# Optimization experiments

Measured on AMD Instinct MI355X. Metric: run time of the kernel, lower is better.

Reference implementation:

```python
import jax, jax.numpy as jnp
import numpy as np

# Dimensions (match init_kwargs / input_specs)
B, CIN, COUT = 4, 8, 32
HIN, WIN = 721, 1440      # input (nlat, nlon)
HOUT, WOUT = 361, 720     # output (nlat, nlon)
K = 9                     # morlet basis: kernel_shape[0]*kernel_shape[1]
NNZ = 32                  # nonzeros per (basis fn, output-lat) row of sparse psi
PSCALE = WIN // WOUT      # longitudinal downsampling factor (must be integer)


def setup_inputs() -> dict:
    key = jax.random.key(0)
    k1, k2, k3, k4, k5 = jax.random.split(key, 5)
    x = jax.random.normal(k1, (B, CIN, HIN, WIN), jnp.float32)
    # Localized sparse support: input lat rows near the matching output lat
    # (emulates the theta_cutoff neighborhood of the precomputed DISCO tensor).
    base_row = jnp.round(jnp.arange(HOUT) * (HIN - 1) / (HOUT - 1)).astype(jnp.int32)
    drow = jax.random.randint(k2, (K, HOUT, NNZ), -2, 3)
    rows = jnp.clip(base_row[None, :, None] + drow, 0, HIN - 1)
    # small longitudinal offsets; the contraction shifts them over all output lons
    cols = jax.random.randint(k3, (K, HOUT, NNZ), 0, 16)
    psi_idx = (rows * WIN + cols).astype(jnp.int32)          # [K, HOUT, NNZ]
    psi_vals = jax.random.normal(k4, (K, HOUT, NNZ), jnp.float32) / NNZ
    weight = jax.random.normal(k5, (COUT, CIN, K), jnp.float32) / np.sqrt(CIN * K)
    return {"x": x, "psi_idx": psi_idx, "psi_vals": psi_vals, "weight": weight}


def _disco_conv(x, psi_idx, psi_vals, weight):
    # DISCO S2 contraction (dense math of torch_harmonics _disco_s2_contraction):
    #   out[b,o,xo,po] = sum_{c,k} weight[o,c,k] * y[b,c,k,xo,po]
    Bv, C, Hin, Win = x.shape
    rows = psi_idx // Win               # [K, Hout, NNZ]
    cols = psi_idx % Win
    x_flat = x.reshape(Bv, C, Hin * Win)

    def step(_, po):
        cols_p = (cols + po * PSCALE) % Win
        idx = rows * Win + cols_p                        # [K,Hout,NNZ]
        xg = x_flat[:, :, idx]                           # [B,C,K,Hout,NNZ] gather
        y_po = jnp.einsum('bckxn,kxn->bckx', xg, psi_vals)
        return None, y_po

    _, y = jax.lax.scan(step, None, jnp.arange(WOUT))    # [Wout,B,C,K,Hout]
    out = jnp.einsum('pbckx,ock->boxp', y, weight)       # [B,Cout,Hout,Wout]
    return out


def reference(x, psi_idx, psi_vals, weight):
    # The wrapper only casts to float32 around the conv; inputs are already fp32.
    return _disco_conv(x.astype(jnp.float32), psi_idx, psi_vals, weight)
```

## Files before the change

kernel.cpp:

```cpp
#include <hip/hip_runtime.h>
#include <hip/hip_bf16.h>

#define HIN   721
#define WIN   1440
#define HOUT_ 361
#define WOUT_ 720
#define NB    4
#define CIN_  8
#define COUT_ 32
#define KT    9
#define NNZ_  32

typedef short  bsh8   __attribute__((ext_vector_type(8)));
typedef float  f32x16 __attribute__((ext_vector_type(16)));
typedef unsigned int u32x4 __attribute__((ext_vector_type(4)));

static __device__ __forceinline__ unsigned short f2bf(float f) {
  unsigned u = __builtin_bit_cast(unsigned, f);
  u += 0x7fffu + ((u >> 16) & 1u);
  return (unsigned short)(u >> 16);
}

static __device__ __forceinline__ unsigned pack2(float a, float b) {
  __hip_bfloat162 h = __float22bfloat162_rn(make_float2(a, b));
  unsigned u; __builtin_memcpy(&u, &h, 4);
  return u;
}

__global__ __launch_bounds__(256) void coeff_kernel(
    const int*   __restrict__ psi_idx,
    const float* __restrict__ psi_vals,
    const float* __restrict__ weight,
    unsigned short* __restrict__ Cg)
{
  __shared__ float Cl[256 * 81];
  __shared__ float wl[COUT_ * CIN_ * KT];
  __shared__ float S[KT][80];

  const int x = blockIdx.x, tid = threadIdx.x;

  for (int i = tid; i < KT * 80; i += 256) ((float*)S)[i] = 0.f;
  for (int i = tid; i < COUT_ * CIN_ * KT; i += 256) wl[i] = weight[i];
  __syncthreads();

  for (int i = tid; i < KT * NNZ_; i += 256) {
    int k = i >> 5, n = i & 31;
    int gi  = (k * HOUT_ + x) * NNZ_ + n;
    int idx = psi_idx[gi];
    int r   = idx / WIN;
    int col = idx - r * WIN;
    int s   = r - 2 * x + 2;
    int slot = (s * 2 + (col & 1)) * 8 + (col >> 1);
    atomicAdd(&S[k][slot], psi_vals[gi]);
  }
  __syncthreads();

  {
    const float* wrow = &wl[tid * KT];
    float w[KT];
    #pragma unroll
    for (int k = 0; k < KT; ++k) w[k] = wrow[k];
    float* seg = &Cl[tid * 81];
    #pragma unroll
    for (int slot = 0; slot < 80; ++slot) {
      float acc = 0.f;
      #pragma unroll
      for (int k = 0; k < KT; ++k) acc += w[k] * S[k][slot];
      seg[slot] = acc;
    }
  }
  __syncthreads();

  for (int chunk = tid; chunk < 8 * 10 * 32; chunk += 256) {
    int j   = chunk / 320;
    int rem = chunk - j * 320;
    int qb  = rem >> 5, o = rem & 31;
    u32x4 pack;
    #pragma unroll
    for (int h = 0; h < 4; ++h) {
      int q0 = qb * 8 + 2 * h;
      int c0 = q0 / 10, ql0 = q0 - c0 * 10;
      int q1 = q0 + 1;
      int c1 = q1 / 10, ql1 = q1 - c1 * 10;
      unsigned lo = f2bf(Cl[(o * CIN_ + c0) * 81 + ql0 * 8 + j]);
      unsigned hi = f2bf(Cl[(o * CIN_ + c1) * 81 + ql1 * 8 + j]);
      pack[h] = lo | (hi << 16);
    }
    *(u32x4*)&Cg[((size_t)x * 2560 + (size_t)((j * 10 + qb) * 32 + o)) * 8] = pack;
  }
}

#define PB   256
#define ROWS 264
#define RST  176

__global__ __launch_bounds__(256, 3) void disco_main_kernel(
    const float* __restrict__ x,
    const unsigned short* __restrict__ Cg,
    float* __restrict__ out)
{
  __shared__ __align__(16) unsigned char Ut[ROWS * RST];

  const int g   = blockIdx.x;
  const int xcd = g & 7, lin = g >> 3;
  const int swz = (xcd < 4) ? xcd * 542 + lin : 4 * 542 + (xcd - 4) * 541 + lin;
  const int xo  = swz / 12;
  const int rem = swz - xo * 12;
  const int pt  = rem % 3;
  const int b   = rem / 3;
  const int p0  = pt * PB;
  const int tid = threadIdx.x;

  const int lane = tid & 63;
  const int wv   = tid >> 6;
  const int half = lane >> 5;
  const int l31  = lane & 31;
  const int wbase = wv * 64;

  const unsigned short* cgx = Cg + (size_t)xo * 2560 * 8
                                 + (size_t)(half * 32 + l31) * 8;

  bsh8 a0[5], a1[5];
  #pragma unroll
  for (int kb = 0; kb < 5; ++kb) a0[kb] = *(const bsh8*)&cgx[kb * 512];
  #pragma unroll
  for (int kb = 0; kb < 5; ++kb) a1[kb] = *(const bsh8*)&cgx[2560 + kb * 512];

  const float* xb = x + (size_t)b * (CIN_ * HIN * WIN);

  int rr[5];
  #pragma unroll
  for (int s = 0; s < 5; ++s) {
    int r = 2 * xo + s - 2;
    rr[s] = r < 0 ? 0 : (r > HIN - 1 ? HIN - 1 : r);
  }

  #pragma unroll
  for (int bp = 0; bp < 2; ++bp) {
    float4 v0[4], v1[4];
    const int uA = tid + (2 * bp) * 256, uB = uA + 256;
    const int chA = uA / 132, rpA = uA - chA * 132;
    const int chB = uB / 132, rpB = uB - chB * 132;
    int cwA = p0 + 2 * rpA; if (cwA >= WOUT_) cwA -= WOUT_;
    int cwB = p0 + 2 * rpB; if (cwB >= WOUT_) cwB -= WOUT_;
    #pragma unroll
    for (int m = 0; m < 4; ++m) {
      int qpA = 4 * chA + m, cA = (qpA * 205) >> 10, sA = qpA - cA * 5;
      v0[m] = *(const float4*)&xb[(size_t)(cA * HIN + rr[sA]) * WIN + 2 * cwA];
      int qpB = 4 * chB + m, cB = (qpB * 205) >> 10, sB = qpB - cB * 5;
      v1[m] = *(const float4*)&xb[(size_t)(cB * HIN + rr[sB]) * WIN + 2 * cwB];
    }
    u32x4 lo, hi;
    #pragma unroll
    for (int m = 0; m < 4; ++m) { lo[m] = pack2(v0[m].x, v0[m].y); hi[m] = pack2(v0[m].z, v0[m].w); }
    int byte0 = (2 * rpA) * RST + chA * 16;
    *(u32x4*)&Ut[byte0]       = lo;
    *(u32x4*)&Ut[byte0 + RST] = hi;
    #pragma unroll
    for (int m = 0; m < 4; ++m) { lo[m] = pack2(v1[m].x, v1[m].y); hi[m] = pack2(v1[m].z, v1[m].w); }
    byte0 = (2 * rpB) * RST + chB * 16;
    *(u32x4*)&Ut[byte0]       = lo;
    *(u32x4*)&Ut[byte0 + RST] = hi;
  }
  {
    const int uA = tid + 1024;
    const int chA = uA / 132, rpA = uA - chA * 132;
    int cwA = p0 + 2 * rpA; if (cwA >= WOUT_) cwA -= WOUT_;
    float4 v0[4], v1[4];
    int chB = 0, rpB = 0;
    const bool tail = tid < 40;
    if (tail) {
      const int uB = tid + 1280;
      chB = uB / 132; rpB = uB - chB * 132;
    }
    int cwB = p0 + 2 * rpB; if (cwB >= WOUT_) cwB -= WOUT_;
    #pragma unroll
    for (int m = 0; m < 4; ++m) {
      int qpA = 4 * chA + m, cA = (qpA * 205) >> 10, sA = qpA - cA * 5;
      v0[m] = *(const float4*)&xb[(size_t)(cA * HIN + rr[sA]) * WIN + 2 * cwA];
    }
    if (tail) {
      #pragma unroll
      for (int m = 0; m < 4; ++m) {
        int qpB = 4 * chB + m, cB = (qpB * 205) >> 10, sB = qpB - cB * 5;
        v1[m] = *(const float4*)&xb[(size_t)(cB * HIN + rr[sB]) * WIN + 2 * cwB];
      }
    }
    u32x4 lo, hi;
    #pragma unroll
    for (int m = 0; m < 4; ++m) { lo[m] = pack2(v0[m].x, v0[m].y); hi[m] = pack2(v0[m].z, v0[m].w); }
    int byte0 = (2 * rpA) * RST + chA * 16;
    *(u32x4*)&Ut[byte0]       = lo;
    *(u32x4*)&Ut[byte0 + RST] = hi;
    if (tail) {
      #pragma unroll
      for (int m = 0; m < 4; ++m) { lo[m] = pack2(v1[m].x, v1[m].y); hi[m] = pack2(v1[m].z, v1[m].w); }
      byte0 = (2 * rpB) * RST + chB * 16;
      *(u32x4*)&Ut[byte0]       = lo;
      *(u32x4*)&Ut[byte0 + RST] = hi;
    }
  }
  __syncthreads();

  f32x16 acc0 = {};
  f32x16 acc1 = {};

  #pragma unroll
  for (int j = 0; j < 8; ++j) {
    bsh8 a2[5];
    if (j < 6) {
      #pragma unroll
      for (int kb = 0; kb < 5; ++kb)
        a2[kb] = *(const bsh8*)&cgx[(j + 2) * 2560 + kb * 512];
    }
    const int row0 = wbase + l31 + j;
    const int rb0  = row0 * RST;
    const int rb1  = rb0 + 32 * RST;
    #pragma unroll
    for (int kb = 0; kb < 5; ++kb) {
      const int cho = (2 * kb + half) * 16;
      bsh8 b0 = *(const bsh8*)&Ut[rb0 + cho];
      acc0 = __builtin_amdgcn_mfma_f32_32x32x16_bf16(a0[kb], b0, acc0, 0, 0, 0);
      bsh8 b1 = *(const bsh8*)&Ut[rb1 + cho];
      acc1 = __builtin_amdgcn_mfma_f32_32x32x16_bf16(a0[kb], b1, acc1, 0, 0, 0);
    }
    #pragma unroll
    for (int kb = 0; kb < 5; ++kb) { a0[kb] = a1[kb]; a1[kb] = a2[kb]; }
  }

  const int p = p0 + wbase + l31;
  #pragma unroll
  for (int r = 0; r < 16; ++r) {
    int o = (r & 3) + 8 * (r >> 2) + 4 * half;
    size_t base = ((size_t)(b * COUT_ + o) * HOUT_ + xo) * WOUT_;
    if (p < WOUT_)
      __builtin_nontemporal_store(acc0[r], &out[base + p]);
    if (p + 32 < WOUT_)
      __builtin_nontemporal_store(acc1[r], &out[base + p + 32]);
  }
}

extern "C" void kernel_launch(void* const* d_in, const int* in_sizes, int n_in,
                              void* d_out, int out_size, void* d_ws, size_t ws_size,
                              hipStream_t stream) {
  const float* x        = (const float*)d_in[0];
  const int*   psi_idx  = (const int*)d_in[1];
  const float* psi_vals = (const float*)d_in[2];
  const float* weight   = (const float*)d_in[3];
  float* out = (float*)d_out;
  unsigned short* Cg = (unsigned short*)d_ws;

  coeff_kernel<<<dim3(HOUT_), 256, 0, stream>>>(psi_idx, psi_vals, weight, Cg);
  disco_main_kernel<<<dim3(3 * NB * HOUT_), 256, 0, stream>>>(x, Cg, out);
}
```

Measured before the change: 93.33 us.

## Split LDS staging into two phases to overlap global loads with MFMA

Splits the K dimension of the staged tile into two parts. The first three k-blocks (channels 0-5) are loaded and stored to LDS, then the loads for the remaining channels are issued before the first MFMA loop, so their global latency hides behind compute. The second half is packed into LDS after the first loop, followed by a barrier and a second MFMA loop. This costs an extra barrier and keeps more loaded values in registers across the first loop, which may hurt occupancy at the 3-blocks-per-SM launch bound.

```diff
diff --git a/kernel.cpp b/kernel.cpp
--- a/kernel.cpp
+++ b/kernel.cpp
@@ -120,11 +120,11 @@
   const unsigned short* cgx = Cg + (size_t)xo * 2560 * 8
                                  + (size_t)(half * 32 + l31) * 8;
 
-  bsh8 a0[5], a1[5];
-  #pragma unroll
-  for (int kb = 0; kb < 5; ++kb) a0[kb] = *(const bsh8*)&cgx[kb * 512];
-  #pragma unroll
-  for (int kb = 0; kb < 5; ++kb) a1[kb] = *(const bsh8*)&cgx[2560 + kb * 512];
+  bsh8 a0[3], a1[3];
+  #pragma unroll
+  for (int kb = 0; kb < 3; ++kb) a0[kb] = *(const bsh8*)&cgx[kb * 512];
+  #pragma unroll
+  for (int kb = 0; kb < 3; ++kb) a1[kb] = *(const bsh8*)&cgx[2560 + kb * 512];
 
   const float* xb = x + (size_t)b * (CIN_ * HIN * WIN);
 
@@ -135,71 +135,92 @@
     rr[s] = r < 0 ? 0 : (r > HIN - 1 ? HIN - 1 : r);
   }
 
-  #pragma unroll
-  for (int bp = 0; bp < 2; ++bp) {
-    float4 v0[4], v1[4];
-    const int uA = tid + (2 * bp) * 256, uB = uA + 256;
-    const int chA = uA / 132, rpA = uA - chA * 132;
-    const int chB = uB / 132, rpB = uB - chB * 132;
-    int cwA = p0 + 2 * rpA; if (cwA >= WOUT_) cwA -= WOUT_;
-    int cwB = p0 + 2 * rpB; if (cwB >= WOUT_) cwB -= WOUT_;
-    #pragma unroll
-    for (int m = 0; m < 4; ++m) {
-      int qpA = 4 * chA + m, cA = (qpA * 205) >> 10, sA = qpA - cA * 5;
-      v0[m] = *(const float4*)&xb[(size_t)(cA * HIN + rr[sA]) * WIN + 2 * cwA];
-      int qpB = 4 * chB + m, cB = (qpB * 205) >> 10, sB = qpB - cB * 5;
-      v1[m] = *(const float4*)&xb[(size_t)(cB * HIN + rr[sB]) * WIN + 2 * cwB];
-    }
-    u32x4 lo, hi;
-    #pragma unroll
-    for (int m = 0; m < 4; ++m) { lo[m] = pack2(v0[m].x, v0[m].y); hi[m] = pack2(v0[m].z, v0[m].w); }
-    int byte0 = (2 * rpA) * RST + chA * 16;
-    *(u32x4*)&Ut[byte0]       = lo;
-    *(u32x4*)&Ut[byte0 + RST] = hi;
-    #pragma unroll
-    for (int m = 0; m < 4; ++m) { lo[m] = pack2(v1[m].x, v1[m].y); hi[m] = pack2(v1[m].z, v1[m].w); }
-    byte0 = (2 * rpB) * RST + chB * 16;
-    *(u32x4*)&Ut[byte0]       = lo;
-    *(u32x4*)&Ut[byte0 + RST] = hi;
-  }
   {
-    const int uA = tid + 1024;
-    const int chA = uA / 132, rpA = uA - chA * 132;
-    int cwA = p0 + 2 * rpA; if (cwA >= WOUT_) cwA -= WOUT_;
-    float4 v0[4], v1[4];
-    int chB = 0, rpB = 0;
-    const bool tail = tid < 40;
-    if (tail) {
-      const int uB = tid + 1280;
-      chB = uB / 132; rpB = uB - chB * 132;
-    }
-    int cwB = p0 + 2 * rpB; if (cwB >= WOUT_) cwB -= WOUT_;
-    #pragma unroll
-    for (int m = 0; m < 4; ++m) {
-      int qpA = 4 * chA + m, cA = (qpA * 205) >> 10, sA = qpA - cA * 5;
-      v0[m] = *(const float4*)&xb[(size_t)(cA * HIN + rr[sA]) * WIN + 2 * cwA];
-    }
-    if (tail) {
+    float4 v[3][4];
+    #pragma unroll
+    for (int pass = 0; pass < 3; ++pass) {
+      const int u  = tid + pass * 256;
+      const int ch = u / 132, rp = u - ch * 132;
+      int cw = p0 + 2 * rp; if (cw >= WOUT_) cw -= WOUT_;
       #pragma unroll
       for (int m = 0; m < 4; ++m) {
-        int qpB = 4 * chB + m, cB = (qpB * 205) >> 10, sB = qpB - cB * 5;
-        v1[m] = *(const float4*)&xb[(size_t)(cB * HIN + rr[sB]) * WIN + 2 * cwB];
+        int qp = 4 * ch + m, c = (qp * 205) >> 10, s = qp - c * 5;
+        v[pass][m] = *(const float4*)&xb[(size_t)(c * HIN + rr[s]) * WIN + 2 * cw];
       }
     }
-    u32x4 lo, hi;
-    #pragma unroll
-    for (int m = 0; m < 4; ++m) { lo[m] = pack2(v0[m].x, v0[m].y); hi[m] = pack2(v0[m].z, v0[m].w); }
-    int byte0 = (2 * rpA) * RST + chA * 16;
-    *(u32x4*)&Ut[byte0]       = lo;
-    *(u32x4*)&Ut[byte0 + RST] = hi;
-    if (tail) {
-      #pragma unroll
-      for (int m = 0; m < 4; ++m) { lo[m] = pack2(v1[m].x, v1[m].y); hi[m] = pack2(v1[m].z, v1[m].w); }
-      byte0 = (2 * rpB) * RST + chB * 16;
+    float4 vt[4];
+    const bool tailA = tid < 24;
+    {
+      const int u  = tailA ? (768 + tid) : 768;
+      const int ch = u / 132, rp = u - ch * 132;
+      int cw = p0 + 2 * rp; if (cw >= WOUT_) cw -= WOUT_;
+      if (tailA) {
+        #pragma unroll
+        for (int m = 0; m < 4; ++m) {
+          int qp = 4 * ch + m, c = (qp * 205) >> 10, s = qp - c * 5;
+          vt[m] = *(const float4*)&xb[(size_t)(c * HIN + rr[s]) * WIN + 2 * cw];
+        }
+      }
+    }
+    #pragma unroll
+    for (int pass = 0; pass < 3; ++pass) {
+      const int u  = tid + pass * 256;
+      const int ch = u / 132, rp = u - ch * 132;
+      u32x4 lo, hi;
+      #pragma unroll
+      for (int m = 0; m < 4; ++m) { lo[m] = pack2(v[pass][m].x, v[pass][m].y);
+                                    hi[m] = pack2(v[pass][m].z, v[pass][m].w); }
+      int byte0 = (2 * rp) * RST + ch * 16;
       *(u32x4*)&Ut[byte0]       = lo;
       *(u32x4*)&Ut[byte0 + RST] = hi;
     }
-  }
+    if (tailA) {
+      const int u  = 768 + tid;
+      const int ch = u / 132, rp = u - ch * 132;
+      u32x4 lo, hi;
+      #pragma unroll
+      for (int m = 0; m < 4; ++m) { lo[m] = pack2(vt[m].x, vt[m].y);
+                                    hi[m] = pack2(vt[m].z, vt[m].w); }
+      int byte0 = (2 * rp) * RST + ch * 16;
+      *(u32x4*)&Ut[byte0]       = lo;
+      *(u32x4*)&Ut[byte0 + RST] = hi;
+    }
+  }
+
+  float4 vB[2][4], vBt[4];
+  int uB[2], uBt;
+  const bool tailB = tid < 16;
+  #pragma unroll
+  for (int pass = 0; pass < 2; ++pass) {
+    const int u  = 792 + tid + pass * 256;
+    uB[pass] = u;
+    const int ch = u / 132, rp = u - ch * 132;
+    int cw = p0 + 2 * rp; if (cw >= WOUT_) cw -= WOUT_;
+    #pragma unroll
+    for (int m = 0; m < 4; ++m) {
+      int qp = 4 * ch + m, c = (qp * 205) >> 10, s = qp - c * 5;
+      vB[pass][m] = *(const float4*)&xb[(size_t)(c * HIN + rr[s]) * WIN + 2 * cw];
+    }
+  }
+  {
+    uBt = tailB ? (1304 + tid) : 1304;
+    const int ch = uBt / 132, rp = uBt - ch * 132;
+    int cw = p0 + 2 * rp; if (cw >= WOUT_) cw -= WOUT_;
+    if (tailB) {
+      #pragma unroll
+      for (int m = 0; m < 4; ++m) {
+        int qp = 4 * ch + m, c = (qp * 205) >> 10, s = qp - c * 5;
+        vBt[m] = *(const float4*)&xb[(size_t)(c * HIN + rr[s]) * WIN + 2 * cw];
+      }
+    }
+  }
+
+  bsh8 c0[2], c1[2];
+  #pragma unroll
+  for (int i = 0; i < 2; ++i) c0[i] = *(const bsh8*)&cgx[(3 + i) * 512];
+  #pragma unroll
+  for (int i = 0; i < 2; ++i) c1[i] = *(const bsh8*)&cgx[2560 + (3 + i) * 512];
+
   __syncthreads();
 
   f32x16 acc0 = {};
@@ -207,17 +228,16 @@
 
   #pragma unroll
   for (int j = 0; j < 8; ++j) {
-    bsh8 a2[5];
+    bsh8 a2[3];
     if (j < 6) {
       #pragma unroll
-      for (int kb = 0; kb < 5; ++kb)
+      for (int kb = 0; kb < 3; ++kb)
         a2[kb] = *(const bsh8*)&cgx[(j + 2) * 2560 + kb * 512];
     }
-    const int row0 = wbase + l31 + j;
-    const int rb0  = row0 * RST;
-    const int rb1  = rb0 + 32 * RST;
-    #pragma unroll
-    for (int kb = 0; kb < 5; ++kb) {
+    const int rb0 = (wbase + l31 + j) * RST;
+    const int rb1 = rb0 + 32 * RST;
+    #pragma unroll
+    for (int kb = 0; kb < 3; ++kb) {
       const int cho = (2 * kb + half) * 16;
       bsh8 b0 = *(const bsh8*)&Ut[rb0 + cho];
       acc0 = __builtin_amdgcn_mfma_f32_32x32x16_bf16(a0[kb], b0, acc0, 0, 0, 0);
@@ -225,7 +245,53 @@
       acc1 = __builtin_amdgcn_mfma_f32_32x32x16_bf16(a0[kb], b1, acc1, 0, 0, 0);
     }
     #pragma unroll
-    for (int kb = 0; kb < 5; ++kb) { a0[kb] = a1[kb]; a1[kb] = a2[kb]; }
+    for (int kb = 0; kb < 3; ++kb) { a0[kb] = a1[kb]; a1[kb] = a2[kb]; }
+  }
+
+  #pragma unroll
+  for (int pass = 0; pass < 2; ++pass) {
+    const int u  = uB[pass];
+    const int ch = u / 132, rp = u - ch * 132;
+    u32x4 lo, hi;
+    #pragma unroll
+    for (int m = 0; m < 4; ++m) { lo[m] = pack2(vB[pass][m].x, vB[pass][m].y);
+                                  hi[m] = pack2(vB[pass][m].z, vB[pass][m].w); }
+    int byte0 = (2 * rp) * RST + ch * 16;
+    *(u32x4*)&Ut[byte0]       = lo;
+    *(u32x4*)&Ut[byte0 + RST] = hi;
+  }
+  if (tailB) {
+    const int ch = uBt / 132, rp = uBt - ch * 132;
+    u32x4 lo, hi;
+    #pragma unroll
+    for (int m = 0; m < 4; ++m) { lo[m] = pack2(vBt[m].x, vBt[m].y);
+                                  hi[m] = pack2(vBt[m].z, vBt[m].w); }
+    int byte0 = (2 * rp) * RST + ch * 16;
+    *(u32x4*)&Ut[byte0]       = lo;
+    *(u32x4*)&Ut[byte0 + RST] = hi;
+  }
+  __syncthreads();
+
+  #pragma unroll
+  for (int j = 0; j < 8; ++j) {
+    bsh8 c2[2];
+    if (j < 6) {
+      #pragma unroll
+      for (int i = 0; i < 2; ++i)
+        c2[i] = *(const bsh8*)&cgx[(j + 2) * 2560 + (3 + i) * 512];
+    }
+    const int rb0 = (wbase + l31 + j) * RST;
+    const int rb1 = rb0 + 32 * RST;
+    #pragma unroll
+    for (int i = 0; i < 2; ++i) {
+      const int cho = (6 + 2 * i + half) * 16;
+      bsh8 b0 = *(const bsh8*)&Ut[rb0 + cho];
+      acc0 = __builtin_amdgcn_mfma_f32_32x32x16_bf16(c0[i], b0, acc0, 0, 0, 0);
+      bsh8 b1 = *(const bsh8*)&Ut[rb1 + cho];
+      acc1 = __builtin_amdgcn_mfma_f32_32x32x16_bf16(c0[i], b1, acc1, 0, 0, 0);
+    }
+    #pragma unroll
+    for (int i = 0; i < 2; ++i) { c0[i] = c1[i]; c1[i] = c2[i]; }
   }
 
   const int p = p0 + wbase + l31;
```

Result: slower. 96.34 us (+3.2%).

## Shrink main kernel to single-wave blocks with private LDS tile, drop barrier

Applied to the files above, without the earlier changes.

Restructures the main kernel from 256-thread blocks covering 256 output longitudes to 64-thread single-wave blocks covering 64 longitudes, each staging its own 72-row bf16 tile in LDS. Because only one wave touches the tile, the block-wide barrier is removed and more, smaller blocks can overlap loads and MFMA across the CU. In exchange, the 8-row halo is reloaded per wave instead of being shared across four waves, which adds redundant global traffic, and the launch has four times as many blocks. The grid swizzle assumes 17328 blocks split evenly across 8 XCDs. Removing the barrier relies on the wave executing its LDS stores and loads in order.

```diff
diff --git a/kernel.cpp b/kernel.cpp
--- a/kernel.cpp
+++ b/kernel.cpp
@@ -90,32 +90,28 @@
   }
 }
 
-#define PB   256
-#define ROWS 264
-#define RST  176
-
-__global__ __launch_bounds__(256, 3) void disco_main_kernel(
+#define WROWS 72
+#define RST   176
+
+__global__ __launch_bounds__(64, 3) void disco_main_kernel(
     const float* __restrict__ x,
     const unsigned short* __restrict__ Cg,
     float* __restrict__ out)
 {
-  __shared__ __align__(16) unsigned char Ut[ROWS * RST];
+  __shared__ __align__(16) unsigned char Ut[WROWS * RST];
 
   const int g   = blockIdx.x;
   const int xcd = g & 7, lin = g >> 3;
-  const int swz = (xcd < 4) ? xcd * 542 + lin : 4 * 542 + (xcd - 4) * 541 + lin;
-  const int xo  = swz / 12;
-  const int rem = swz - xo * 12;
-  const int pt  = rem % 3;
-  const int b   = rem / 3;
-  const int p0  = pt * PB;
-  const int tid = threadIdx.x;
-
-  const int lane = tid & 63;
-  const int wv   = tid >> 6;
+  const int swz = xcd * 2166 + lin;
+  const int xo  = swz / 48;
+  const int rem = swz - xo * 48;
+  const int b   = rem / 12;
+  const int pw  = rem - b * 12;
+  const int po  = pw * 64;
+
+  const int lane = threadIdx.x;
   const int half = lane >> 5;
   const int l31  = lane & 31;
-  const int wbase = wv * 64;
 
   const unsigned short* cgx = Cg + (size_t)xo * 2560 * 8
                                  + (size_t)(half * 32 + l31) * 8;
@@ -135,72 +131,80 @@
     rr[s] = r < 0 ? 0 : (r > HIN - 1 ? HIN - 1 : r);
   }
 
-  #pragma unroll
-  for (int bp = 0; bp < 2; ++bp) {
-    float4 v0[4], v1[4];
-    const int uA = tid + (2 * bp) * 256, uB = uA + 256;
-    const int chA = uA / 132, rpA = uA - chA * 132;
-    const int chB = uB / 132, rpB = uB - chB * 132;
-    int cwA = p0 + 2 * rpA; if (cwA >= WOUT_) cwA -= WOUT_;
-    int cwB = p0 + 2 * rpB; if (cwB >= WOUT_) cwB -= WOUT_;
-    #pragma unroll
-    for (int m = 0; m < 4; ++m) {
-      int qpA = 4 * chA + m, cA = (qpA * 205) >> 10, sA = qpA - cA * 5;
-      v0[m] = *(const float4*)&xb[(size_t)(cA * HIN + rr[sA]) * WIN + 2 * cwA];
-      int qpB = 4 * chB + m, cB = (qpB * 205) >> 10, sB = qpB - cB * 5;
-      v1[m] = *(const float4*)&xb[(size_t)(cB * HIN + rr[sB]) * WIN + 2 * cwB];
-    }
-    u32x4 lo, hi;
-    #pragma unroll
-    for (int m = 0; m < 4; ++m) { lo[m] = pack2(v0[m].x, v0[m].y); hi[m] = pack2(v0[m].z, v0[m].w); }
-    int byte0 = (2 * rpA) * RST + chA * 16;
-    *(u32x4*)&Ut[byte0]       = lo;
-    *(u32x4*)&Ut[byte0 + RST] = hi;
-    #pragma unroll
-    for (int m = 0; m < 4; ++m) { lo[m] = pack2(v1[m].x, v1[m].y); hi[m] = pack2(v1[m].z, v1[m].w); }
-    byte0 = (2 * rpB) * RST + chB * 16;
-    *(u32x4*)&Ut[byte0]       = lo;
-    *(u32x4*)&Ut[byte0 + RST] = hi;
-  }
   {
-    const int uA = tid + 1024;
-    const int chA = uA / 132, rpA = uA - chA * 132;
-    int cwA = p0 + 2 * rpA; if (cwA >= WOUT_) cwA -= WOUT_;
-    float4 v0[4], v1[4];
-    int chB = 0, rpB = 0;
-    const bool tail = tid < 40;
-    if (tail) {
-      const int uB = tid + 1280;
-      chB = uB / 132; rpB = uB - chB * 132;
-    }
-    int cwB = p0 + 2 * rpB; if (cwB >= WOUT_) cwB -= WOUT_;
-    #pragma unroll
-    for (int m = 0; m < 4; ++m) {
-      int qpA = 4 * chA + m, cA = (qpA * 205) >> 10, sA = qpA - cA * 5;
-      v0[m] = *(const float4*)&xb[(size_t)(cA * HIN + rr[sA]) * WIN + 2 * cwA];
-    }
-    if (tail) {
+    float4 v[3][4];
+    #pragma unroll
+    for (int k = 0; k < 3; ++k) {
+      const int u  = lane + k * 64;
+      const int ch = u / 36, rp = u - ch * 36;
+      int cw = po + 2 * rp; if (cw >= WOUT_) cw -= WOUT_;
       #pragma unroll
       for (int m = 0; m < 4; ++m) {
-        int qpB = 4 * chB + m, cB = (qpB * 205) >> 10, sB = qpB - cB * 5;
-        v1[m] = *(const float4*)&xb[(size_t)(cB * HIN + rr[sB]) * WIN + 2 * cwB];
+        int qp = 4 * ch + m, c = (qp * 205) >> 10, s = qp - c * 5;
+        v[k][m] = *(const float4*)&xb[(size_t)(c * HIN + rr[s]) * WIN + 2 * cw];
       }
     }
-    u32x4 lo, hi;
-    #pragma unroll
-    for (int m = 0; m < 4; ++m) { lo[m] = pack2(v0[m].x, v0[m].y); hi[m] = pack2(v0[m].z, v0[m].w); }
-    int byte0 = (2 * rpA) * RST + chA * 16;
-    *(u32x4*)&Ut[byte0]       = lo;
-    *(u32x4*)&Ut[byte0 + RST] = hi;
-    if (tail) {
-      #pragma unroll
-      for (int m = 0; m < 4; ++m) { lo[m] = pack2(v1[m].x, v1[m].y); hi[m] = pack2(v1[m].z, v1[m].w); }
-      byte0 = (2 * rpB) * RST + chB * 16;
+    #pragma unroll
+    for (int k = 0; k < 3; ++k) {
+      const int u  = lane + k * 64;
+      const int ch = u / 36, rp = u - ch * 36;
+      u32x4 lo, hi;
+      #pragma unroll
+      for (int m = 0; m < 4; ++m) { lo[m] = pack2(v[k][m].x, v[k][m].y);
+                                    hi[m] = pack2(v[k][m].z, v[k][m].w); }
+      const int byte0 = (2 * rp) * RST + ch * 16;
       *(u32x4*)&Ut[byte0]       = lo;
       *(u32x4*)&Ut[byte0 + RST] = hi;
     }
   }
-  __syncthreads();
+  {
+    float4 v[2][4], vt[4];
+    const bool tl = lane < 40;
+    #pragma unroll
+    for (int k = 0; k < 2; ++k) {
+      const int u  = lane + (3 + k) * 64;
+      const int ch = u / 36, rp = u - ch * 36;
+      int cw = po + 2 * rp; if (cw >= WOUT_) cw -= WOUT_;
+      #pragma unroll
+      for (int m = 0; m < 4; ++m) {
+        int qp = 4 * ch + m, c = (qp * 205) >> 10, s = qp - c * 5;
+        v[k][m] = *(const float4*)&xb[(size_t)(c * HIN + rr[s]) * WIN + 2 * cw];
+      }
+    }
+    if (tl) {
+      const int u  = 320 + lane;
+      const int ch = u / 36, rp = u - ch * 36;
+      int cw = po + 2 * rp; if (cw >= WOUT_) cw -= WOUT_;
+      #pragma unroll
+      for (int m = 0; m < 4; ++m) {
+        int qp = 4 * ch + m, c = (qp * 205) >> 10, s = qp - c * 5;
+        vt[m] = *(const float4*)&xb[(size_t)(c * HIN + rr[s]) * WIN + 2 * cw];
+      }
+    }
+    #pragma unroll
+    for (int k = 0; k < 2; ++k) {
+      const int u  = lane + (3 + k) * 64;
+      const int ch = u / 36, rp = u - ch * 36;
+      u32x4 lo, hi;
+      #pragma unroll
+      for (int m = 0; m < 4; ++m) { lo[m] = pack2(v[k][m].x, v[k][m].y);
+                                    hi[m] = pack2(v[k][m].z, v[k][m].w); }
+      const int byte0 = (2 * rp) * RST + ch * 16;
+      *(u32x4*)&Ut[byte0]       = lo;
+      *(u32x4*)&Ut[byte0 + RST] = hi;
+    }
+    if (tl) {
+      const int u  = 320 + lane;
+      const int ch = u / 36, rp = u - ch * 36;
+      u32x4 lo, hi;
+      #pragma unroll
+      for (int m = 0; m < 4; ++m) { lo[m] = pack2(vt[m].x, vt[m].y);
+                                    hi[m] = pack2(vt[m].z, vt[m].w); }
+      const int byte0 = (2 * rp) * RST + ch * 16;
+      *(u32x4*)&Ut[byte0]       = lo;
+      *(u32x4*)&Ut[byte0 + RST] = hi;
+    }
+  }
 
   f32x16 acc0 = {};
   f32x16 acc1 = {};
@@ -213,9 +217,8 @@
       for (int kb = 0; kb < 5; ++kb)
         a2[kb] = *(const bsh8*)&cgx[(j + 2) * 2560 + kb * 512];
     }
-    const int row0 = wbase + l31 + j;
-    const int rb0  = row0 * RST;
-    const int rb1  = rb0 + 32 * RST;
+    const int rb0 = (l31 + j) * RST;
+    const int rb1 = rb0 + 32 * RST;
     #pragma unroll
     for (int kb = 0; kb < 5; ++kb) {
       const int cho = (2 * kb + half) * 16;
@@ -228,7 +231,7 @@
     for (int kb = 0; kb < 5; ++kb) { a0[kb] = a1[kb]; a1[kb] = a2[kb]; }
   }
 
-  const int p = p0 + wbase + l31;
+  const int p = po + l31;
   #pragma unroll
   for (int r = 0; r < 16; ++r) {
     int o = (r & 3) + 8 * (r >> 2) + 4 * half;
@@ -251,5 +254,5 @@
   unsigned short* Cg = (unsigned short*)d_ws;
 
   coeff_kernel<<<dim3(HOUT_), 256, 0, stream>>>(psi_idx, psi_vals, weight, Cg);
-  disco_main_kernel<<<dim3(3 * NB * HOUT_), 256, 0, stream>>>(x, Cg, out);
-}
+  disco_main_kernel<<<dim3(12 * NB * HOUT_), 64, 0, stream>>>(x, Cg, out);
+}
```

New measurement: 97.62 us. +4.6%, slower.

## Loop longitude tiles inside each block and shrink coeff kernel shared memory

Applied to the files above, without the earlier changes.

The main kernel now launches one block per (output latitude, batch) and runs the three longitude tiles in a loop inside the block, with a barrier between tiles that reuse the same LDS buffer. This cuts block count and launch/scheduling overhead, and lets repeated coefficient loads hit cache. The cost is fewer blocks and less parallelism, plus serialized tiles with no overlap of loads and MFMA. The coeff kernel also stores bf16 coefficients in LDS and reads weights straight into registers, shrinking shared memory so more blocks can be resident.

```diff
diff --git a/kernel.cpp b/kernel.cpp
--- a/kernel.cpp
+++ b/kernel.cpp
@@ -27,20 +27,18 @@
   return u;
 }
 
-__global__ __launch_bounds__(256) void coeff_kernel(
+__global__ __launch_bounds__(256, 3) void coeff_kernel(
     const int*   __restrict__ psi_idx,
     const float* __restrict__ psi_vals,
     const float* __restrict__ weight,
     unsigned short* __restrict__ Cg)
 {
-  __shared__ float Cl[256 * 81];
-  __shared__ float wl[COUT_ * CIN_ * KT];
+  __shared__ unsigned short Cl16[256 * 83];
   __shared__ float S[KT][80];
 
   const int x = blockIdx.x, tid = threadIdx.x;
 
   for (int i = tid; i < KT * 80; i += 256) ((float*)S)[i] = 0.f;
-  for (int i = tid; i < COUT_ * CIN_ * KT; i += 256) wl[i] = weight[i];
   __syncthreads();
 
   for (int i = tid; i < KT * NNZ_; i += 256) {
@@ -53,20 +51,20 @@
     int slot = (s * 2 + (col & 1)) * 8 + (col >> 1);
     atomicAdd(&S[k][slot], psi_vals[gi]);
   }
+
+  float w[KT];
+  #pragma unroll
+  for (int k = 0; k < KT; ++k) w[k] = weight[tid * KT + k];
   __syncthreads();
 
   {
-    const float* wrow = &wl[tid * KT];
-    float w[KT];
-    #pragma unroll
-    for (int k = 0; k < KT; ++k) w[k] = wrow[k];
-    float* seg = &Cl[tid * 81];
+    unsigned short* seg = &Cl16[tid * 83];
     #pragma unroll
     for (int slot = 0; slot < 80; ++slot) {
       float acc = 0.f;
       #pragma unroll
       for (int k = 0; k < KT; ++k) acc += w[k] * S[k][slot];
-      seg[slot] = acc;
+      seg[slot] = f2bf(acc);
     }
   }
   __syncthreads();
@@ -82,8 +80,8 @@
       int c0 = q0 / 10, ql0 = q0 - c0 * 10;
       int q1 = q0 + 1;
       int c1 = q1 / 10, ql1 = q1 - c1 * 10;
-      unsigned lo = f2bf(Cl[(o * CIN_ + c0) * 81 + ql0 * 8 + j]);
-      unsigned hi = f2bf(Cl[(o * CIN_ + c1) * 81 + ql1 * 8 + j]);
+      unsigned lo = Cl16[(o * CIN_ + c0) * 83 + ql0 * 8 + j];
+      unsigned hi = Cl16[(o * CIN_ + c1) * 83 + ql1 * 8 + j];
       pack[h] = lo | (hi << 16);
     }
     *(u32x4*)&Cg[((size_t)x * 2560 + (size_t)((j * 10 + qb) * 32 + o)) * 8] = pack;
@@ -103,12 +101,9 @@
 
   const int g   = blockIdx.x;
   const int xcd = g & 7, lin = g >> 3;
-  const int swz = (xcd < 4) ? xcd * 542 + lin : 4 * 542 + (xcd - 4) * 541 + lin;
-  const int xo  = swz / 12;
-  const int rem = swz - xo * 12;
-  const int pt  = rem % 3;
-  const int b   = rem / 3;
-  const int p0  = pt * PB;
+  const int swz = (xcd < 4) ? xcd * 181 + lin : 724 + (xcd - 4) * 180 + lin;
+  const int xo  = swz >> 2;
+  const int b   = swz & 3;
   const int tid = threadIdx.x;
 
   const int lane = tid & 63;
@@ -119,13 +114,6 @@
 
   const unsigned short* cgx = Cg + (size_t)xo * 2560 * 8
                                  + (size_t)(half * 32 + l31) * 8;
-
-  bsh8 a0[5], a1[5];
-  #pragma unroll
-  for (int kb = 0; kb < 5; ++kb) a0[kb] = *(const bsh8*)&cgx[kb * 512];
-  #pragma unroll
-  for (int kb = 0; kb < 5; ++kb) a1[kb] = *(const bsh8*)&cgx[2560 + kb * 512];
-
   const float* xb = x + (size_t)b * (CIN_ * HIN * WIN);
 
   int rr[5];
@@ -135,108 +123,118 @@
     rr[s] = r < 0 ? 0 : (r > HIN - 1 ? HIN - 1 : r);
   }
 
-  #pragma unroll
-  for (int bp = 0; bp < 2; ++bp) {
-    float4 v0[4], v1[4];
-    const int uA = tid + (2 * bp) * 256, uB = uA + 256;
-    const int chA = uA / 132, rpA = uA - chA * 132;
-    const int chB = uB / 132, rpB = uB - chB * 132;
-    int cwA = p0 + 2 * rpA; if (cwA >= WOUT_) cwA -= WOUT_;
-    int cwB = p0 + 2 * rpB; if (cwB >= WOUT_) cwB -= WOUT_;
-    #pragma unroll
-    for (int m = 0; m < 4; ++m) {
-      int qpA = 4 * chA + m, cA = (qpA * 205) >> 10, sA = qpA - cA * 5;
-      v0[m] = *(const float4*)&xb[(size_t)(cA * HIN + rr[sA]) * WIN + 2 * cwA];
-      int qpB = 4 * chB + m, cB = (qpB * 205) >> 10, sB = qpB - cB * 5;
-      v1[m] = *(const float4*)&xb[(size_t)(cB * HIN + rr[sB]) * WIN + 2 * cwB];
-    }
-    u32x4 lo, hi;
-    #pragma unroll
-    for (int m = 0; m < 4; ++m) { lo[m] = pack2(v0[m].x, v0[m].y); hi[m] = pack2(v0[m].z, v0[m].w); }
-    int byte0 = (2 * rpA) * RST + chA * 16;
-    *(u32x4*)&Ut[byte0]       = lo;
-    *(u32x4*)&Ut[byte0 + RST] = hi;
-    #pragma unroll
-    for (int m = 0; m < 4; ++m) { lo[m] = pack2(v1[m].x, v1[m].y); hi[m] = pack2(v1[m].z, v1[m].w); }
-    byte0 = (2 * rpB) * RST + chB * 16;
-    *(u32x4*)&Ut[byte0]       = lo;
-    *(u32x4*)&Ut[byte0 + RST] = hi;
-  }
-  {
-    const int uA = tid + 1024;
-    const int chA = uA / 132, rpA = uA - chA * 132;
-    int cwA = p0 + 2 * rpA; if (cwA >= WOUT_) cwA -= WOUT_;
-    float4 v0[4], v1[4];
-    int chB = 0, rpB = 0;
-    const bool tail = tid < 40;
-    if (tail) {
-      const int uB = tid + 1280;
-      chB = uB / 132; rpB = uB - chB * 132;
-    }
-    int cwB = p0 + 2 * rpB; if (cwB >= WOUT_) cwB -= WOUT_;
-    #pragma unroll
-    for (int m = 0; m < 4; ++m) {
-      int qpA = 4 * chA + m, cA = (qpA * 205) >> 10, sA = qpA - cA * 5;
-      v0[m] = *(const float4*)&xb[(size_t)(cA * HIN + rr[sA]) * WIN + 2 * cwA];
-    }
-    if (tail) {
+  for (int pt = 0; pt < 3; ++pt) {
+    const int p0 = pt * PB;
+    if (pt) __syncthreads();
+
+    bsh8 a0[5], a1[5];
+    #pragma unroll
+    for (int kb = 0; kb < 5; ++kb) a0[kb] = *(const bsh8*)&cgx[kb * 512];
+    #pragma unroll
+    for (int kb = 0; kb < 5; ++kb) a1[kb] = *(const bsh8*)&cgx[2560 + kb * 512];
+
+    #pragma unroll
+    for (int bp = 0; bp < 2; ++bp) {
+      float4 v0[4], v1[4];
+      const int uA = tid + (2 * bp) * 256, uB = uA + 256;
+      const int chA = uA / 132, rpA = uA - chA * 132;
+      const int chB = uB / 132, rpB = uB - chB * 132;
+      int cwA = p0 + 2 * rpA; if (cwA >= WOUT_) cwA -= WOUT_;
+      int cwB = p0 + 2 * rpB; if (cwB >= WOUT_) cwB -= WOUT_;
       #pragma unroll
       for (int m = 0; m < 4; ++m) {
+        int qpA = 4 * chA + m, cA = (qpA * 205) >> 10, sA = qpA - cA * 5;
+        v0[m] = *(const float4*)&xb[(size_t)(cA * HIN + rr[sA]) * WIN + 2 * cwA];
         int qpB = 4 * chB + m, cB = (qpB * 205) >> 10, sB = qpB - cB * 5;
         v1[m] = *(const float4*)&xb[(size_t)(cB * HIN + rr[sB]) * WIN + 2 * cwB];
       }
-    }
-    u32x4 lo, hi;
-    #pragma unroll
-    for (int m = 0; m < 4; ++m) { lo[m] = pack2(v0[m].x, v0[m].y); hi[m] = pack2(v0[m].z, v0[m].w); }
-    int byte0 = (2 * rpA) * RST + chA * 16;
-    *(u32x4*)&Ut[byte0]       = lo;
-    *(u32x4*)&Ut[byte0 + RST] = hi;
-    if (tail) {
+      u32x4 lo, hi;
+      #pragma unroll
+      for (int m = 0; m < 4; ++m) { lo[m] = pack2(v0[m].x, v0[m].y); hi[m] = pack2(v0[m].z, v0[m].w); }
+      int byte0 = (2 * rpA) * RST + chA * 16;
+      *(u32x4*)&Ut[byte0]       = lo;
+      *(u32x4*)&Ut[byte0 + RST] = hi;
       #pragma unroll
       for (int m = 0; m < 4; ++m) { lo[m] = pack2(v1[m].x, v1[m].y); hi[m] = pack2(v1[m].z, v1[m].w); }
       byte0 = (2 * rpB) * RST + chB * 16;
       *(u32x4*)&Ut[byte0]       = lo;
       *(u32x4*)&Ut[byte0 + RST] = hi;
     }
-  }
-  __syncthreads();
-
-  f32x16 acc0 = {};
-  f32x16 acc1 = {};
-
-  #pragma unroll
-  for (int j = 0; j < 8; ++j) {
-    bsh8 a2[5];
-    if (j < 6) {
-      #pragma unroll
-      for (int kb = 0; kb < 5; ++kb)
-        a2[kb] = *(const bsh8*)&cgx[(j + 2) * 2560 + kb * 512];
-    }
-    const int row0 = wbase + l31 + j;
-    const int rb0  = row0 * RST;
-    const int rb1  = rb0 + 32 * RST;
-    #pragma unroll
-    for (int kb = 0; kb < 5; ++kb) {
-      const int cho = (2 * kb + half) * 16;
-      bsh8 b0 = *(const bsh8*)&Ut[rb0 + cho];
-      acc0 = __builtin_amdgcn_mfma_f32_32x32x16_bf16(a0[kb], b0, acc0, 0, 0, 0);
-      bsh8 b1 = *(const bsh8*)&Ut[rb1 + cho];
-      acc1 = __builtin_amdgcn_mfma_f32_32x32x16_bf16(a0[kb], b1, acc1, 0, 0, 0);
-    }
-    #pragma unroll
-    for (int kb = 0; kb < 5; ++kb) { a0[kb] = a1[kb]; a1[kb] = a2[kb]; }
-  }
-
-  const int p = p0 + wbase + l31;
-  #pragma unroll
-  for (int r = 0; r < 16; ++r) {
-    int o = (r & 3) + 8 * (r >> 2) + 4 * half;
-    size_t base = ((size_t)(b * COUT_ + o) * HOUT_ + xo) * WOUT_;
-    if (p < WOUT_)
-      __builtin_nontemporal_store(acc0[r], &out[base + p]);
-    if (p + 32 < WOUT_)
-      __builtin_nontemporal_store(acc1[r], &out[base + p + 32]);
+    {
+      const int uA = tid + 1024;
+      const int chA = uA / 132, rpA = uA - chA * 132;
+      int cwA = p0 + 2 * rpA; if (cwA >= WOUT_) cwA -= WOUT_;
+      float4 v0[4], v1[4];
+      int chB = 0, rpB = 0;
+      const bool tail = tid < 40;
+      if (tail) {
+        const int uB = tid + 1280;
+        chB = uB / 132; rpB = uB - chB * 132;
+      }
+      int cwB = p0 + 2 * rpB; if (cwB >= WOUT_) cwB -= WOUT_;
+      #pragma unroll
+      for (int m = 0; m < 4; ++m) {
+        int qpA = 4 * chA + m, cA = (qpA * 205) >> 10, sA = qpA - cA * 5;
+        v0[m] = *(const float4*)&xb[(size_t)(cA * HIN + rr[sA]) * WIN + 2 * cwA];
+      }
+      if (tail) {
+        #pragma unroll
+        for (int m = 0; m < 4; ++m) {
+          int qpB = 4 * chB + m, cB = (qpB * 205) >> 10, sB = qpB - cB * 5;
+          v1[m] = *(const float4*)&xb[(size_t)(cB * HIN + rr[sB]) * WIN + 2 * cwB];
+        }
+      }
+      u32x4 lo, hi;
+      #pragma unroll
+      for (int m = 0; m < 4; ++m) { lo[m] = pack2(v0[m].x, v0[m].y); hi[m] = pack2(v0[m].z, v0[m].w); }
+      int byte0 = (2 * rpA) * RST + chA * 16;
+      *(u32x4*)&Ut[byte0]       = lo;
+      *(u32x4*)&Ut[byte0 + RST] = hi;
+      if (tail) {
+        #pragma unroll
+        for (int m = 0; m < 4; ++m) { lo[m] = pack2(v1[m].x, v1[m].y); hi[m] = pack2(v1[m].z, v1[m].w); }
+        byte0 = (2 * rpB) * RST + chB * 16;
+        *(u32x4*)&Ut[byte0]       = lo;
+        *(u32x4*)&Ut[byte0 + RST] = hi;
+      }
+    }
+    __syncthreads();
+
+    f32x16 acc0 = {};
+    f32x16 acc1 = {};
+
+    #pragma unroll
+    for (int j = 0; j < 8; ++j) {
+      bsh8 a2[5];
+      if (j < 6) {
+        #pragma unroll
+        for (int kb = 0; kb < 5; ++kb)
+          a2[kb] = *(const bsh8*)&cgx[(j + 2) * 2560 + kb * 512];
+      }
+      const int rb0 = (wbase + l31 + j) * RST;
+      const int rb1 = rb0 + 32 * RST;
+      #pragma unroll
+      for (int kb = 0; kb < 5; ++kb) {
+        const int cho = (2 * kb + half) * 16;
+        bsh8 b0 = *(const bsh8*)&Ut[rb0 + cho];
+        acc0 = __builtin_amdgcn_mfma_f32_32x32x16_bf16(a0[kb], b0, acc0, 0, 0, 0);
+        bsh8 b1 = *(const bsh8*)&Ut[rb1 + cho];
+        acc1 = __builtin_amdgcn_mfma_f32_32x32x16_bf16(a0[kb], b1, acc1, 0, 0, 0);
+      }
+      #pragma unroll
+      for (int kb = 0; kb < 5; ++kb) { a0[kb] = a1[kb]; a1[kb] = a2[kb]; }
+    }
+
+    const int p = p0 + wbase + l31;
+    #pragma unroll
+    for (int r = 0; r < 16; ++r) {
+      int o = (r & 3) + 8 * (r >> 2) + 4 * half;
+      size_t base = ((size_t)(b * COUT_ + o) * HOUT_ + xo) * WOUT_;
+      if (p < WOUT_)
+        __builtin_nontemporal_store(acc0[r], &out[base + p]);
+      if (p + 32 < WOUT_)
+        __builtin_nontemporal_store(acc1[r], &out[base + p + 32]);
+    }
   }
 }
 
@@ -251,5 +249,5 @@
   unsigned short* Cg = (unsigned short*)d_ws;
 
   coeff_kernel<<<dim3(HOUT_), 256, 0, stream>>>(psi_idx, psi_vals, weight, Cg);
-  disco_main_kernel<<<dim3(3 * NB * HOUT_), 256, 0, stream>>>(x, Cg, out);
-}
+  disco_main_kernel<<<dim3(4 * HOUT_), 256, 0, stream>>>(x, Cg, out);
+}
```

After: 198.4 us. 2.13x slower.
